# Optimization experiments

Hardware: AMD Instinct MI355X
Metric: run time of the kernel (lower is better)

The kernel has to match this reference:

```python
import jax, jax.numpy as jnp
import numpy as np

N_NODES = 100000


def _deg_norm(idx, n):
    # inverse-sqrt degree, zero-degree nodes -> 0 (DGL norm='both' convention)
    deg = jax.ops.segment_sum(jnp.ones(idx.shape, jnp.float32), idx, num_segments=n)
    return jnp.where(deg > 0, jax.lax.rsqrt(jnp.maximum(deg, 1.0)), 0.0)


def graph_conv(x, src, dst, W, b, n):
    # symmetric normalization: D_out^{-1/2} on src, D_in^{-1/2} on dst
    norm_src = _deg_norm(src, n)  # [N]
    norm_dst = _deg_norm(dst, n)  # [N]
    h = (x * norm_src[:, None]) @ W          # apply weight first (in >= out)
    msg = h[src]                              # gather [E, out]
    agg = jax.ops.segment_sum(msg, dst, num_segments=n)  # scatter-add [N, out]
    return agg * norm_dst[:, None] + b


def setup_inputs() -> dict:
    key = jax.random.key(0)
    ks = jax.random.split(key, 6)
    x = jax.random.normal(ks[0], (N_NODES, 128), dtype=jnp.float32)
    edge_index = jax.random.randint(ks[1], (2, 1600000), 0, N_NODES, dtype=jnp.int64)
    W1 = jax.random.normal(ks[2], (128, 64), dtype=jnp.float32) * (1.0 / np.sqrt(128))
    b1 = jnp.zeros((64,), jnp.float32)
    W2 = jax.random.normal(ks[3], (64, 32), dtype=jnp.float32) * (1.0 / np.sqrt(64))
    b2 = jnp.zeros((32,), jnp.float32)
    Wl = jax.random.normal(ks[4], (32, 1), dtype=jnp.float32) * (1.0 / np.sqrt(32))
    bl = jnp.zeros((1,), jnp.float32)
    return {"x": x, "edge_index": edge_index, "W1": W1, "b1": b1,
            "W2": W2, "b2": b2, "Wl": Wl, "bl": bl}


def reference(x, edge_index, W1, b1, W2, b2, Wl, bl):
    src, dst = edge_index[0], edge_index[1]
    n = x.shape[0]
    h = graph_conv(x, src, dst, W1, b1, n)
    h = jax.nn.relu(h)
    # dropout(p=0.5) is identity at inference
    h = graph_conv(h, src, dst, W2, b2, n)
    return h @ Wl + bl  # [N, 1]
```

## Files before the change

### kernel.cpp

```cpp
#include <hip/hip_runtime.h>
#include <hip/hip_fp16.h>


#define WAVE 64
#define NRANGE 8
#define NPAIR 4

typedef _Float16 f16x8 __attribute__((ext_vector_type(8)));
typedef float f32x4 __attribute__((ext_vector_type(4)));

__global__ __launch_bounds__(256) void k_hist(const int* __restrict__ srcArr,
                                              const int* __restrict__ dstArr,
                                              unsigned* __restrict__ partial_s,
                                              unsigned* __restrict__ partial_d,
                                              int E, int B, int C, int chunkE) {
    extern __shared__ unsigned hist[];
    const int pr = blockIdx.x & (NPAIR - 1);
    const int c = blockIdx.x >> 2;
    const int lo = pr * 2 * B;
    const int* nodes = blockIdx.y ? dstArr : srcArr;
    unsigned* partial = blockIdx.y ? partial_d : partial_s;

    for (int b = threadIdx.x; b < B; b += 256) hist[b] = 0u;
    __syncthreads();

    const int beg = c * chunkE, end = min(beg + chunkE, E);
    const int n4 = (end - beg) >> 2;
    const int4* p = (const int4*)(nodes + beg);
    for (int j = threadIdx.x; j < n4; j += 256) {
        int4 v = p[j];
        int a;
        a = v.x - lo; if ((unsigned)a < (unsigned)(2 * B)) { int h = a >= B; atomicAdd(&hist[a - (h ? B : 0)], h ? 0x10000u : 1u); }
        a = v.y - lo; if ((unsigned)a < (unsigned)(2 * B)) { int h = a >= B; atomicAdd(&hist[a - (h ? B : 0)], h ? 0x10000u : 1u); }
        a = v.z - lo; if ((unsigned)a < (unsigned)(2 * B)) { int h = a >= B; atomicAdd(&hist[a - (h ? B : 0)], h ? 0x10000u : 1u); }
        a = v.w - lo; if ((unsigned)a < (unsigned)(2 * B)) { int h = a >= B; atomicAdd(&hist[a - (h ? B : 0)], h ? 0x10000u : 1u); }
    }
    for (int j = beg + (n4 << 2) + threadIdx.x; j < end; j += 256) {
        int a = nodes[j] - lo;
        if ((unsigned)a < (unsigned)(2 * B)) { int h = a >= B; atomicAdd(&hist[a - (h ? B : 0)], h ? 0x10000u : 1u); }
    }
    __syncthreads();
    unsigned* outp = partial + (size_t)(pr * C + c) * B;
    for (int b = threadIdx.x; b < B; b += 256) outp[b] = hist[b];
}

__global__ __launch_bounds__(256) void k_reduce_norm(const unsigned* __restrict__ partial_s,
                                                     unsigned* __restrict__ partial_d,
                                                     float* __restrict__ norm_s,
                                                     float* __restrict__ norm_d,
                                                     unsigned* __restrict__ deg_d,
                                                     int N, int B, int C) {
    int t = blockIdx.x * 256 + threadIdx.x;
    if (t >= NPAIR * B) return;
    int pr = t / B, b = t - pr * B;
    int n0 = pr * 2 * B + b, n1 = n0 + B;
    size_t base = (size_t)(pr * C) * B + b;
    unsigned ds = 0;
    for (int c = 0; c < C; ++c) ds += partial_s[base + (size_t)c * B];
    unsigned run = 0;
    for (int c = 0; c < C; ++c) {
        size_t ix = base + (size_t)c * B;
        unsigned v = partial_d[ix];
        partial_d[ix] = run;
        run += v;
    }
    unsigned ds0 = ds & 0xffffu, ds1 = ds >> 16;
    unsigned dd0 = run & 0xffffu, dd1 = run >> 16;
    if (n0 < N) {
        deg_d[n0] = dd0;
        norm_s[n0] = ds0 ? rsqrtf((float)ds0) : 0.0f;
        norm_d[n0] = dd0 ? rsqrtf((float)dd0) : 0.0f;
    }
    if (n1 < N) {
        deg_d[n1] = dd1;
        norm_s[n1] = ds1 ? rsqrtf((float)ds1) : 0.0f;
        norm_d[n1] = dd1 ? rsqrtf((float)dd1) : 0.0f;
    }
}

__global__ void k_w2l(const float* __restrict__ W2, const float* __restrict__ b2,
                      const float* __restrict__ Wl, const float* __restrict__ bl,
                      float* __restrict__ w2l, float* __restrict__ c0) {
    int c = threadIdx.x;
    float acc = 0.f;
#pragma unroll
    for (int j = 0; j < 32; ++j) acc += W2[c * 32 + j] * Wl[j];
    w2l[c] = acc;
    if (c == 0) {
        float s = 0.f;
#pragma unroll
        for (int j = 0; j < 32; ++j) s += b2[j] * Wl[j];
        *c0 = s + bl[0];
    }
}

__global__ __launch_bounds__(256) void k_wt(const float* __restrict__ W1,
                                            _Float16* __restrict__ wt) {
    int t = threadIdx.x;
    for (int i = 0; i < 32; ++i) {
        int e = i * 256 + t;
        int k = e >> 6, n = e & 63;
        wt[n * 128 + k] = (_Float16)W1[e];
    }
}

__global__ __launch_bounds__(256) void k_blocksum(const unsigned* __restrict__ deg,
                                                  unsigned* __restrict__ partial, int N) {
    __shared__ unsigned sw[4];
    int i = blockIdx.x * 256 + threadIdx.x;
    unsigned v = (i < N) ? deg[i] : 0u;
#pragma unroll
    for (int off = 32; off; off >>= 1) v += __shfl_xor((int)v, off);
    if ((threadIdx.x & 63) == 0) sw[threadIdx.x >> 6] = v;
    __syncthreads();
    if (threadIdx.x == 0) partial[blockIdx.x] = sw[0] + sw[1] + sw[2] + sw[3];
}

__global__ __launch_bounds__(512) void k_scanpartial(const unsigned* __restrict__ partial,
                                                     unsigned* __restrict__ blockoff,
                                                     unsigned* __restrict__ offsets,
                                                     int nb, int N) {
    __shared__ unsigned s[512];
    int t = threadIdx.x;
    unsigned v = (t < nb) ? partial[t] : 0u;
    s[t] = v;
    __syncthreads();
    for (int off = 1; off < 512; off <<= 1) {
        unsigned a = (t >= off) ? s[t - off] : 0u;
        __syncthreads();
        s[t] += a;
        __syncthreads();
    }
    if (t < nb) blockoff[t] = s[t] - v;
    if (t == nb - 1) offsets[N] = s[t];
}

__global__ __launch_bounds__(256) void k_offsets(const unsigned* __restrict__ deg,
                                                 const unsigned* __restrict__ blockoff,
                                                 unsigned* __restrict__ offsets, int N) {
    __shared__ unsigned s[256];
    int t = threadIdx.x;
    int i = blockIdx.x * 256 + t;
    unsigned v = (i < N) ? deg[i] : 0u;
    s[t] = v;
    __syncthreads();
    for (int off = 1; off < 256; off <<= 1) {
        unsigned a = (t >= off) ? s[t - off] : 0u;
        __syncthreads();
        s[t] += a;
        __syncthreads();
    }
    if (i < N) offsets[i] = blockoff[blockIdx.x] + s[t] - v;
}

__global__ __launch_bounds__(256) void k_fill(const int* __restrict__ src,
                                              const int* __restrict__ dst,
                                              const unsigned* __restrict__ offsets,
                                              const unsigned* __restrict__ rel,
                                              unsigned* __restrict__ csr,
                                              int N, int E, int B, int C, int chunkE) {
    extern __shared__ unsigned curs[];
    const int r = blockIdx.x & (NRANGE - 1);
    const int c = blockIdx.x >> 3;
    const int lo = r * B;
    const int bins = min(B, N - lo);
    const int pr = r >> 1, hs = (r & 1) << 4;
    const unsigned* relp = rel + (size_t)(pr * C + c) * B;
    for (int b = threadIdx.x; b < bins; b += 256)
        curs[b] = offsets[lo + b] + ((relp[b] >> hs) & 0xffffu);
    __syncthreads();

    const int beg = c * chunkE, end = min(beg + chunkE, E);
    const int n4 = (end - beg) >> 2;
    const int4* pd = (const int4*)(dst + beg);
    const int4* ps = (const int4*)(src + beg);
    for (int j = threadIdx.x; j < n4; j += 256) {
        int4 d4 = pd[j];
        int4 s4 = ps[j];
        int a;
        a = d4.x - lo; if ((unsigned)a < (unsigned)bins) csr[atomicAdd(&curs[a], 1u)] = (unsigned)s4.x;
        a = d4.y - lo; if ((unsigned)a < (unsigned)bins) csr[atomicAdd(&curs[a], 1u)] = (unsigned)s4.y;
        a = d4.z - lo; if ((unsigned)a < (unsigned)bins) csr[atomicAdd(&curs[a], 1u)] = (unsigned)s4.z;
        a = d4.w - lo; if ((unsigned)a < (unsigned)bins) csr[atomicAdd(&curs[a], 1u)] = (unsigned)s4.w;
    }
    for (int j = beg + (n4 << 2) + threadIdx.x; j < end; j += 256) {
        int a = dst[j] - lo;
        if ((unsigned)a < (unsigned)bins) csr[atomicAdd(&curs[a], 1u)] = (unsigned)src[j];
    }
}

__global__ __launch_bounds__(256) void k_gemm1(const float* __restrict__ x,
                                               const _Float16* __restrict__ wt,
                                               const float* __restrict__ norm_s,
                                               __half* __restrict__ h1h, int N) {
    __shared__ __align__(16) _Float16 xs[64 * 128];
    const int tid = threadIdx.x, lane = tid & 63, wv = tid >> 6;
    const int r0 = blockIdx.x * 64;

    f16x8 bf[4][4];
#pragma unroll
    for (int kt = 0; kt < 4; ++kt)
#pragma unroll
        for (int nt = 0; nt < 4; ++nt)
            bf[kt][nt] = *(const f16x8*)&wt[(nt * 16 + (lane & 15)) * 128 +
                                            kt * 32 + (lane >> 4) * 8];

#pragma unroll
    for (int it = 0; it < 8; ++it) {
        int e = it * 256 + tid;
        int r = e >> 5, c = e & 31;
        int row = r0 + r;
        float4 v = (row < N) ? ((const float4*)x)[(size_t)row * 32 + c]
                             : make_float4(0.f, 0.f, 0.f, 0.f);
        __half2 lo2 = __floats2half2_rn(v.x, v.y);
        __half2 hi2 = __floats2half2_rn(v.z, v.w);
        uint2 pk;
        pk.x = *(unsigned*)&lo2;
        pk.y = *(unsigned*)&hi2;
        int byte = r * 256 + c * 8;
        byte ^= (r & 7) << 4;
        *(uint2*)((char*)xs + byte) = pk;
    }
    __syncthreads();

    f32x4 acc[4] = {};
    const int rloc = wv * 16 + (lane & 15);
#pragma unroll
    for (int kt = 0; kt < 4; ++kt) {
        int byte = rloc * 256 + (kt * 32 + (lane >> 4) * 8) * 2;
        byte ^= (rloc & 7) << 4;
        f16x8 af = *(const f16x8*)((char*)xs + byte);
#pragma unroll
        for (int nt = 0; nt < 4; ++nt)
            acc[nt] = __builtin_amdgcn_mfma_f32_16x16x32_f16(af, bf[kt][nt], acc[nt], 0, 0, 0);
    }

#pragma unroll
    for (int j = 0; j < 4; ++j) {
        int row = r0 + wv * 16 + (lane >> 4) * 4 + j;
        if (row < N) {
            float ns = norm_s[row];
#pragma unroll
            for (int nt = 0; nt < 4; ++nt)
                h1h[(size_t)row * 64 + nt * 16 + (lane & 15)] =
                    __float2half(acc[nt][j] * ns);
        }
    }
}

__global__ __launch_bounds__(256) void k_agg_rdot(const unsigned* __restrict__ offsets,
                                                  const unsigned* __restrict__ csr,
                                                  const __half* __restrict__ h1h,
                                                  const float* __restrict__ norm_s,
                                                  const float* __restrict__ norm_d,
                                                  const float* __restrict__ b1,
                                                  const float* __restrict__ w2l,
                                                  float* __restrict__ s_node, int N) {
    const int lane = threadIdx.x & 63;
    const int slot = lane >> 5;
    const int p = lane & 31;
    const int v = (blockIdx.x * 256 + threadIdx.x) >> 6;
    if (v >= N) return;
    const unsigned beg = offsets[v], end = offsets[v + 1];

    float ax = 0.f, ay = 0.f;
    unsigned i = beg;
    for (; i + 8 <= end; i += 8) {
        int s0 = (int)csr[i + 0 + slot];
        int s1 = (int)csr[i + 2 + slot];
        int s2 = (int)csr[i + 4 + slot];
        int s3 = (int)csr[i + 6 + slot];
        unsigned u0 = *(const unsigned*)&h1h[(size_t)s0 * 64 + 2 * p];
        unsigned u1 = *(const unsigned*)&h1h[(size_t)s1 * 64 + 2 * p];
        unsigned u2 = *(const unsigned*)&h1h[(size_t)s2 * 64 + 2 * p];
        unsigned u3 = *(const unsigned*)&h1h[(size_t)s3 * 64 + 2 * p];
        float2 f0 = __half22float2(*(__half2*)&u0);
        float2 f1 = __half22float2(*(__half2*)&u1);
        float2 f2 = __half22float2(*(__half2*)&u2);
        float2 f3 = __half22float2(*(__half2*)&u3);
        ax += (f0.x + f1.x) + (f2.x + f3.x);
        ay += (f0.y + f1.y) + (f2.y + f3.y);
    }
    for (; i < end; i += 2) {
        unsigned e = i + slot;
        if (e < end) {
            int s = (int)csr[e];
            unsigned u = *(const unsigned*)&h1h[(size_t)s * 64 + 2 * p];
            float2 f = __half22float2(*(__half2*)&u);
            ax += f.x; ay += f.y;
        }
    }
    ax += __shfl_xor(ax, 32);
    ay += __shfl_xor(ay, 32);

    float nd = norm_d[v];
    float t = fmaxf(fmaf(ax, nd, b1[2 * p]), 0.f) * w2l[2 * p]
            + fmaxf(fmaf(ay, nd, b1[2 * p + 1]), 0.f) * w2l[2 * p + 1];
#pragma unroll
    for (int off = 16; off; off >>= 1) t += __shfl_xor(t, off);
    if (lane == 0) s_node[v] = t * norm_s[v];
}

__global__ __launch_bounds__(256) void k_out(const unsigned* __restrict__ offsets,
                                             const unsigned* __restrict__ csr,
                                             const float* __restrict__ s_node,
                                             const float* __restrict__ norm_d,
                                             const float* __restrict__ c0,
                                             float* __restrict__ out, int N) {
    int v = blockIdx.x * 256 + threadIdx.x;
    if (v >= N) return;
    unsigned beg = offsets[v], end = offsets[v + 1];
    float sum = 0.f;
    unsigned j = beg;
    for (; j + 4 <= end; j += 4) {
        float a = s_node[csr[j + 0]], b = s_node[csr[j + 1]];
        float c = s_node[csr[j + 2]], d = s_node[csr[j + 3]];
        sum += a + b + c + d;
    }
    for (; j < end; ++j) sum += s_node[csr[j]];
    out[v] = fmaf(sum, norm_d[v], *c0);
}

extern "C" void kernel_launch(void* const* d_in, const int* in_sizes, int n_in,
                              void* d_out, int out_size, void* d_ws, size_t ws_size,
                              hipStream_t stream) {
    const float* x  = (const float*)d_in[0];
    const int*   ei = (const int*)d_in[1];
    const float* W1 = (const float*)d_in[2];
    const float* b1 = (const float*)d_in[3];
    const float* W2 = (const float*)d_in[4];
    const float* b2 = (const float*)d_in[5];
    const float* Wl = (const float*)d_in[6];
    const float* bl = (const float*)d_in[7];

    const int N = in_sizes[0] / 128;
    const int E = in_sizes[1] / 2;
    const int* src = ei;
    const int* dst = ei + E;
    const int NB = (N + 255) / 256;
    const int B = (N + NRANGE - 1) / NRANGE;

    size_t baseBytes = 0;
    {
        auto pad = [](size_t b) { return (b + 255) & ~(size_t)255; };
        baseBytes = pad((size_t)N * 4) * 3 + pad((size_t)(N + 1) * 4) +
                    pad((size_t)NB * 4) * 2 + pad((size_t)N * 64 * 2) +
                    pad((size_t)E * 4) + pad((size_t)N * 4) + pad(64 * 4) + pad(4) +
                    pad(64 * 128 * 2);
    }
    int C = 32;
    while (C > 4 && baseBytes + 2ull * NPAIR * C * B * 4ull > ws_size) C >>= 1;
    const int chunkE = (((E + C - 1) / C) + 3) & ~3;

    char* w = (char*)d_ws;
    auto alloc = [&](size_t bytes) -> void* {
        void* r = (void*)w;
        w += (bytes + 255) & ~(size_t)255;
        return r;
    };
    float*    norm_s    = (float*)alloc((size_t)N * 4);
    float*    norm_d    = (float*)alloc((size_t)N * 4);
    unsigned* deg_d     = (unsigned*)alloc((size_t)N * 4);
    unsigned* offsets   = (unsigned*)alloc((size_t)(N + 1) * 4);
    unsigned* partial   = (unsigned*)alloc((size_t)NB * 4);
    unsigned* blockoff  = (unsigned*)alloc((size_t)NB * 4);
    __half*   h1h       = (__half*)alloc((size_t)N * 64 * 2);
    unsigned* csr       = (unsigned*)alloc((size_t)E * 4);
    float*    s_node    = (float*)alloc((size_t)N * 4);
    float*    w2l       = (float*)alloc(64 * 4);
    float*    c0        = (float*)alloc(4);
    _Float16* wt        = (_Float16*)alloc(64 * 128 * 2);
    unsigned* partial_s = (unsigned*)alloc((size_t)NPAIR * C * B * 4);
    unsigned* partial_d = (unsigned*)alloc((size_t)NPAIR * C * B * 4);

    float* out = (float*)d_out;
    const size_t ldsB = (size_t)B * 4;

    k_hist<<<dim3(NPAIR * C, 2), 256, ldsB, stream>>>(src, dst, partial_s, partial_d,
                                                      E, B, C, chunkE);
    k_w2l<<<1, 64, 0, stream>>>(W2, b2, Wl, bl, w2l, c0);
    k_wt<<<1, 256, 0, stream>>>(W1, wt);
    k_reduce_norm<<<(NPAIR * B + 255) / 256, 256, 0, stream>>>(partial_s, partial_d,
                                                               norm_s, norm_d,
                                                               deg_d, N, B, C);

    k_blocksum<<<NB, 256, 0, stream>>>(deg_d, partial, N);
    k_scanpartial<<<1, 512, 0, stream>>>(partial, blockoff, offsets, NB, N);
    k_offsets<<<NB, 256, 0, stream>>>(deg_d, blockoff, offsets, N);

    k_fill<<<NRANGE * C, 256, ldsB, stream>>>(src, dst, offsets, partial_d, csr,
                                              N, E, B, C, chunkE);

    k_gemm1<<<(N + 63) / 64, 256, 0, stream>>>(x, wt, norm_s, h1h, N);

    k_agg_rdot<<<(N + 3) / 4, 256, 0, stream>>>(offsets, csr, h1h, norm_s, norm_d,
                                                b1, w2l, s_node, N);
    k_out<<<NB, 256, 0, stream>>>(offsets, csr, s_node, norm_d, c0, out, N);
}
```

Baseline: 204.1 us.

## Pre-bucket edges by destination range before CSR fill; stage neighbor indices via shuffles

Adds a bucketing pass that partitions edges by destination range per chunk, using histogram counts computed in k_hist and a small scan. The fill kernel then reads only its own bucket instead of every block rescanning all edges of its chunk and discarding most of them. The aggregation kernel now loads 64 CSR indices per wave at once and broadcasts them with shuffles, unrolled 16-wide. This trades the eight-fold redundant edge reads for one extra write and read of an 8-byte-per-edge buffer, plus two more kernel launches.

```diff
diff --git a/kernel.cpp b/kernel.cpp
--- a/kernel.cpp
+++ b/kernel.cpp
@@ -13,8 +13,10 @@
                                               const int* __restrict__ dstArr,
                                               unsigned* __restrict__ partial_s,
                                               unsigned* __restrict__ partial_d,
+                                              unsigned* __restrict__ cnt,
                                               int E, int B, int C, int chunkE) {
     extern __shared__ unsigned hist[];
+    __shared__ unsigned red[8];
     const int pr = blockIdx.x & (NPAIR - 1);
     const int c = blockIdx.x >> 2;
     const int lo = pr * 2 * B;
@@ -41,7 +43,29 @@
     }
     __syncthreads();
     unsigned* outp = partial + (size_t)(pr * C + c) * B;
-    for (int b = threadIdx.x; b < B; b += 256) outp[b] = hist[b];
+    unsigned slo = 0, shi = 0;
+    for (int b = threadIdx.x; b < B; b += 256) {
+        unsigned h = hist[b];
+        outp[b] = h;
+        slo += h & 0xffffu;
+        shi += h >> 16;
+    }
+    if (blockIdx.y == 1) {
+#pragma unroll
+        for (int off = 32; off; off >>= 1) {
+            slo += __shfl_xor((int)slo, off);
+            shi += __shfl_xor((int)shi, off);
+        }
+        if ((threadIdx.x & 63) == 0) {
+            red[(threadIdx.x >> 6) * 2] = slo;
+            red[(threadIdx.x >> 6) * 2 + 1] = shi;
+        }
+        __syncthreads();
+        if (threadIdx.x == 0) {
+            cnt[(2 * pr) * C + c]     = red[0] + red[2] + red[4] + red[6];
+            cnt[(2 * pr + 1) * C + c] = red[1] + red[3] + red[5] + red[7];
+        }
+    }
 }
 
 __global__ __launch_bounds__(256) void k_reduce_norm(const unsigned* __restrict__ partial_s,
@@ -153,12 +177,68 @@
     if (i < N) offsets[i] = blockoff[blockIdx.x] + s[t] - v;
 }
 
-__global__ __launch_bounds__(256) void k_fill(const int* __restrict__ src,
-                                              const int* __restrict__ dst,
-                                              const unsigned* __restrict__ offsets,
-                                              const unsigned* __restrict__ rel,
-                                              unsigned* __restrict__ csr,
-                                              int N, int E, int B, int C, int chunkE) {
+__global__ __launch_bounds__(256) void k_scancnt(const unsigned* __restrict__ cnt,
+                                                 unsigned* __restrict__ segBase, int nseg) {
+    __shared__ unsigned s[256];
+    int t = threadIdx.x;
+    unsigned v = (t < nseg) ? cnt[t] : 0u;
+    s[t] = v;
+    __syncthreads();
+    for (int off = 1; off < 256; off <<= 1) {
+        unsigned a = (t >= off) ? s[t - off] : 0u;
+        __syncthreads();
+        s[t] += a;
+        __syncthreads();
+    }
+    if (t < nseg) segBase[t] = s[t] - v;
+}
+
+__global__ __launch_bounds__(256) void k_bucket(const int* __restrict__ src,
+                                                const int* __restrict__ dst,
+                                                const unsigned* __restrict__ segBase,
+                                                uint2* __restrict__ ebuf,
+                                                int E, int B, int C, int chunkE) {
+    __shared__ unsigned lcnt[NRANGE];
+    const int c = blockIdx.x;
+    const int lane = threadIdx.x & 63;
+    if (threadIdx.x < NRANGE) lcnt[threadIdx.x] = 0u;
+    __syncthreads();
+
+    unsigned sb[NRANGE];
+#pragma unroll
+    for (int r = 0; r < NRANGE; ++r) sb[r] = segBase[r * C + c];
+
+    const int beg = c * chunkE, end = min(beg + chunkE, E);
+    for (int i = beg + (int)threadIdx.x; i < end; i += 256) {
+        int d = dst[i];
+        int s = src[i];
+        int r4 = (d >= 4 * B) ? 4 : 0;
+        int r2 = (d >= (r4 + 2) * B) ? 2 : 0;
+        int r = r4 + r2 + ((d >= (r4 + r2 + 1) * B) ? 1 : 0);
+#pragma unroll
+        for (int rr = 0; rr < NRANGE; ++rr) {
+            unsigned long long m = __ballot(r == rr);
+            if (m) {
+                int leader = __ffsll((long long)m) - 1;
+                unsigned base = 0;
+                if (lane == leader) base = atomicAdd(&lcnt[rr], (unsigned)__popcll(m));
+                base = (unsigned)__shfl((int)base, leader);
+                if (r == rr) {
+                    unsigned before = (unsigned)__popcll(m & ((1ull << lane) - 1ull));
+                    ebuf[sb[rr] + base + before] = make_uint2((unsigned)s, (unsigned)d);
+                }
+            }
+        }
+    }
+}
+
+__global__ __launch_bounds__(256) void k_fill2(const uint2* __restrict__ ebuf,
+                                               const unsigned* __restrict__ segBase,
+                                               const unsigned* __restrict__ cnt,
+                                               const unsigned* __restrict__ offsets,
+                                               const unsigned* __restrict__ rel,
+                                               unsigned* __restrict__ csr,
+                                               int N, int B, int C) {
     extern __shared__ unsigned curs[];
     const int r = blockIdx.x & (NRANGE - 1);
     const int c = blockIdx.x >> 3;
@@ -170,22 +250,13 @@
         curs[b] = offsets[lo + b] + ((relp[b] >> hs) & 0xffffu);
     __syncthreads();
 
-    const int beg = c * chunkE, end = min(beg + chunkE, E);
-    const int n4 = (end - beg) >> 2;
-    const int4* pd = (const int4*)(dst + beg);
-    const int4* ps = (const int4*)(src + beg);
-    for (int j = threadIdx.x; j < n4; j += 256) {
-        int4 d4 = pd[j];
-        int4 s4 = ps[j];
-        int a;
-        a = d4.x - lo; if ((unsigned)a < (unsigned)bins) csr[atomicAdd(&curs[a], 1u)] = (unsigned)s4.x;
-        a = d4.y - lo; if ((unsigned)a < (unsigned)bins) csr[atomicAdd(&curs[a], 1u)] = (unsigned)s4.y;
-        a = d4.z - lo; if ((unsigned)a < (unsigned)bins) csr[atomicAdd(&curs[a], 1u)] = (unsigned)s4.z;
-        a = d4.w - lo; if ((unsigned)a < (unsigned)bins) csr[atomicAdd(&curs[a], 1u)] = (unsigned)s4.w;
-    }
-    for (int j = beg + (n4 << 2) + threadIdx.x; j < end; j += 256) {
-        int a = dst[j] - lo;
-        if ((unsigned)a < (unsigned)bins) csr[atomicAdd(&curs[a], 1u)] = (unsigned)src[j];
+    const unsigned s0 = segBase[r * C + c];
+    const unsigned len = cnt[r * C + c];
+    for (unsigned i = s0 + threadIdx.x; i < s0 + len; i += 256) {
+        uint2 e = ebuf[i];
+        int a = (int)e.y - lo;
+        if ((unsigned)a < (unsigned)bins)
+            csr[atomicAdd(&curs[a], 1u)] = e.x;
     }
 }
 
@@ -264,30 +335,62 @@
     const unsigned beg = offsets[v], end = offsets[v + 1];
 
     float ax = 0.f, ay = 0.f;
-    unsigned i = beg;
-    for (; i + 8 <= end; i += 8) {
-        int s0 = (int)csr[i + 0 + slot];
-        int s1 = (int)csr[i + 2 + slot];
-        int s2 = (int)csr[i + 4 + slot];
-        int s3 = (int)csr[i + 6 + slot];
-        unsigned u0 = *(const unsigned*)&h1h[(size_t)s0 * 64 + 2 * p];
-        unsigned u1 = *(const unsigned*)&h1h[(size_t)s1 * 64 + 2 * p];
-        unsigned u2 = *(const unsigned*)&h1h[(size_t)s2 * 64 + 2 * p];
-        unsigned u3 = *(const unsigned*)&h1h[(size_t)s3 * 64 + 2 * p];
-        float2 f0 = __half22float2(*(__half2*)&u0);
-        float2 f1 = __half22float2(*(__half2*)&u1);
-        float2 f2 = __half22float2(*(__half2*)&u2);
-        float2 f3 = __half22float2(*(__half2*)&u3);
-        ax += (f0.x + f1.x) + (f2.x + f3.x);
-        ay += (f0.y + f1.y) + (f2.y + f3.y);
-    }
-    for (; i < end; i += 2) {
-        unsigned e = i + slot;
-        if (e < end) {
-            int s = (int)csr[e];
-            unsigned u = *(const unsigned*)&h1h[(size_t)s * 64 + 2 * p];
-            float2 f = __half22float2(*(__half2*)&u);
-            ax += f.x; ay += f.y;
+    for (unsigned base = beg; base < end; base += WAVE) {
+        const int n = (int)min((unsigned)WAVE, end - base);
+        int sv = (lane < n) ? (int)csr[base + lane] : 0;
+        int i = 0;
+        for (; i + 16 <= n; i += 16) {
+            int s0 = __shfl(sv, i + 0 + slot);
+            int s1 = __shfl(sv, i + 2 + slot);
+            int s2 = __shfl(sv, i + 4 + slot);
+            int s3 = __shfl(sv, i + 6 + slot);
+            int s4 = __shfl(sv, i + 8 + slot);
+            int s5 = __shfl(sv, i + 10 + slot);
+            int s6 = __shfl(sv, i + 12 + slot);
+            int s7 = __shfl(sv, i + 14 + slot);
+            unsigned u0 = *(const unsigned*)&h1h[(size_t)s0 * 64 + 2 * p];
+            unsigned u1 = *(const unsigned*)&h1h[(size_t)s1 * 64 + 2 * p];
+            unsigned u2 = *(const unsigned*)&h1h[(size_t)s2 * 64 + 2 * p];
+            unsigned u3 = *(const unsigned*)&h1h[(size_t)s3 * 64 + 2 * p];
+            unsigned u4 = *(const unsigned*)&h1h[(size_t)s4 * 64 + 2 * p];
+            unsigned u5 = *(const unsigned*)&h1h[(size_t)s5 * 64 + 2 * p];
+            unsigned u6 = *(const unsigned*)&h1h[(size_t)s6 * 64 + 2 * p];
+            unsigned u7 = *(const unsigned*)&h1h[(size_t)s7 * 64 + 2 * p];
+            float2 f0 = __half22float2(*(__half2*)&u0);
+            float2 f1 = __half22float2(*(__half2*)&u1);
+            float2 f2 = __half22float2(*(__half2*)&u2);
+            float2 f3 = __half22float2(*(__half2*)&u3);
+            float2 f4 = __half22float2(*(__half2*)&u4);
+            float2 f5 = __half22float2(*(__half2*)&u5);
+            float2 f6 = __half22float2(*(__half2*)&u6);
+            float2 f7 = __half22float2(*(__half2*)&u7);
+            ax += ((f0.x + f1.x) + (f2.x + f3.x)) + ((f4.x + f5.x) + (f6.x + f7.x));
+            ay += ((f0.y + f1.y) + (f2.y + f3.y)) + ((f4.y + f5.y) + (f6.y + f7.y));
+        }
+        for (; i + 8 <= n; i += 8) {
+            int s0 = __shfl(sv, i + 0 + slot);
+            int s1 = __shfl(sv, i + 2 + slot);
+            int s2 = __shfl(sv, i + 4 + slot);
+            int s3 = __shfl(sv, i + 6 + slot);
+            unsigned u0 = *(const unsigned*)&h1h[(size_t)s0 * 64 + 2 * p];
+            unsigned u1 = *(const unsigned*)&h1h[(size_t)s1 * 64 + 2 * p];
+            unsigned u2 = *(const unsigned*)&h1h[(size_t)s2 * 64 + 2 * p];
+            unsigned u3 = *(const unsigned*)&h1h[(size_t)s3 * 64 + 2 * p];
+            float2 f0 = __half22float2(*(__half2*)&u0);
+            float2 f1 = __half22float2(*(__half2*)&u1);
+            float2 f2 = __half22float2(*(__half2*)&u2);
+            float2 f3 = __half22float2(*(__half2*)&u3);
+            ax += (f0.x + f1.x) + (f2.x + f3.x);
+            ay += (f0.y + f1.y) + (f2.y + f3.y);
+        }
+        for (; i < n; i += 2) {
+            int e = i + slot;
+            int s = __shfl(sv, min(e, n - 1));
+            if (e < n) {
+                unsigned u = *(const unsigned*)&h1h[(size_t)s * 64 + 2 * p];
+                float2 f = __half22float2(*(__half2*)&u);
+                ax += f.x; ay += f.y;
+            }
         }
     }
     ax += __shfl_xor(ax, 32);
@@ -346,11 +449,12 @@
         baseBytes = pad((size_t)N * 4) * 3 + pad((size_t)(N + 1) * 4) +
                     pad((size_t)NB * 4) * 2 + pad((size_t)N * 64 * 2) +
                     pad((size_t)E * 4) + pad((size_t)N * 4) + pad(64 * 4) + pad(4) +
-                    pad(64 * 128 * 2);
+                    pad(64 * 128 * 2) + pad((size_t)E * 8) + pad(256 * 4) * 2;
     }
     int C = 32;
     while (C > 4 && baseBytes + 2ull * NPAIR * C * B * 4ull > ws_size) C >>= 1;
     const int chunkE = (((E + C - 1) / C) + 3) & ~3;
+    const int nseg = NRANGE * C;
 
     char* w = (char*)d_ws;
     auto alloc = [&](size_t bytes) -> void* {
@@ -370,6 +474,9 @@
     float*    w2l       = (float*)alloc(64 * 4);
     float*    c0        = (float*)alloc(4);
     _Float16* wt        = (_Float16*)alloc(64 * 128 * 2);
+    uint2*    ebuf      = (uint2*)alloc((size_t)E * 8);
+    unsigned* cnt       = (unsigned*)alloc(256 * 4);
+    unsigned* segBase   = (unsigned*)alloc(256 * 4);
     unsigned* partial_s = (unsigned*)alloc((size_t)NPAIR * C * B * 4);
     unsigned* partial_d = (unsigned*)alloc((size_t)NPAIR * C * B * 4);
 
@@ -377,19 +484,21 @@
     const size_t ldsB = (size_t)B * 4;
 
     k_hist<<<dim3(NPAIR * C, 2), 256, ldsB, stream>>>(src, dst, partial_s, partial_d,
-                                                      E, B, C, chunkE);
+                                                      cnt, E, B, C, chunkE);
     k_w2l<<<1, 64, 0, stream>>>(W2, b2, Wl, bl, w2l, c0);
     k_wt<<<1, 256, 0, stream>>>(W1, wt);
+    k_scancnt<<<1, 256, 0, stream>>>(cnt, segBase, nseg);
+    k_bucket<<<C, 256, 0, stream>>>(src, dst, segBase, ebuf, E, B, C, chunkE);
+
     k_reduce_norm<<<(NPAIR * B + 255) / 256, 256, 0, stream>>>(partial_s, partial_d,
                                                                norm_s, norm_d,
                                                                deg_d, N, B, C);
-
     k_blocksum<<<NB, 256, 0, stream>>>(deg_d, partial, N);
     k_scanpartial<<<1, 512, 0, stream>>>(partial, blockoff, offsets, NB, N);
     k_offsets<<<NB, 256, 0, stream>>>(deg_d, blockoff, offsets, N);
 
-    k_fill<<<NRANGE * C, 256, ldsB, stream>>>(src, dst, offsets, partial_d, csr,
-                                              N, E, B, C, chunkE);
+    k_fill2<<<nseg, 256, ldsB, stream>>>(ebuf, segBase, cnt, offsets, partial_d,
+                                         csr, N, B, C);
 
     k_gemm1<<<(N + 63) / 64, 256, 0, stream>>>(x, wt, norm_s, h1h, N);
 
```

Result: slower. 464.1 us (+127.4%).
